# Kernel optimization log

Measured on AMD Instinct MI355X. Metric: run time of the kernel, lower is better.

Reference implementation:

```python
import jax, jax.numpy as jnp
import numpy as np

VOCAB = 100000
E = 300          # embedding_size
S = 128          # seq_len
B = 8192         # batch
H1 = 2048
H2 = 2048
C = 1221         # num_classes
PAD = 1          # padding token id (sentence trimmed after last non-1 token)


def setup_inputs() -> dict:
    key = jax.random.key(0)
    ks = jax.random.split(key, 8)
    x = jax.random.randint(ks[0], (S, B), 0, VOCAB, dtype=jnp.int64 if jax.config.jax_enable_x64 else jnp.int32)
    emb = jax.random.normal(ks[1], (VOCAB, E), dtype=jnp.float32) * 0.1
    W1 = jax.random.normal(ks[2], (H1, 2 * E), dtype=jnp.float32) * (1.0 / np.sqrt(2 * E))
    b1 = jnp.zeros((H1,), dtype=jnp.float32)
    W2 = jax.random.normal(ks[3], (H2, H1), dtype=jnp.float32) * (1.0 / np.sqrt(H1))
    b2 = jnp.zeros((H2,), dtype=jnp.float32)
    W_out = jax.random.normal(ks[4], (C, H2), dtype=jnp.float32) * (1.0 / np.sqrt(H2))
    b_out = jnp.zeros((C,), dtype=jnp.float32)
    return {"x": x, "emb": emb, "W1": W1, "b1": b1, "W2": W2, "b2": b2,
            "W_out": W_out, "b_out": b_out}


def reference(x, emb, W1, b1, W2, b2, W_out, b_out):
    # x: [S, B] token ids -> transpose to [B, S] as in torch forward
    xb = x.T                                   # [B, S]
    nonpad = xb != PAD                         # [B, S]
    # index of LAST non-padding token per sentence (torch: (sent != 1).nonzero()[-1])
    last = (S - 1) - jnp.argmax(nonpad[:, ::-1], axis=1)      # [B]
    pos = jnp.arange(S)
    # sentence[:last+1] keeps everything up to and including `last`,
    # including any PAD tokens inside that prefix (faithful to the slice).
    mask = (pos[None, :] <= last[:, None]).astype(emb.dtype)  # [B, S]

    ex = emb[xb]                               # [B, S, E] embedding lookup
    mean = jnp.einsum('bse,bs->be', ex, mask) / jnp.sum(mask, axis=1, keepdims=True)
    feat = jnp.concatenate([ex[:, 0, :], mean], axis=1)       # [B, 2E] (FEE + avg)

    h = jax.nn.relu(feat @ W1.T + b1)          # [B, H1]
    h = jax.nn.relu(h @ W2.T + b2)             # [B, H2]
    out = h @ W_out.T + b_out                  # [B, C]
    return out
```

## Files before the change

### kernel.cpp

```cpp
#include <hip/hip_runtime.h>
#include <hip/hip_bf16.h>

#define S 128
#define BATCH 8192
#define E 300
#define KPAD 640
#define H1 2048
#define H2 2048
#define CLS 1221
#define CPAD 1280
#define PADTOK 1
#define VOCAB 100000

typedef __bf16 bf16x8 __attribute__((ext_vector_type(8)));
typedef float f32x4 __attribute__((ext_vector_type(4)));

__device__ __forceinline__ float b2f(ushort u) {
  union { unsigned int i; float f; } v; v.i = ((unsigned int)u) << 16; return v.f;
}
__device__ __forceinline__ ushort f2b(float f) {
  unsigned int i = __float_as_uint(f);
  unsigned int r = (i + 0x7FFFu + ((i >> 16) & 1u)) >> 16;
  return (ushort)r;
}
__device__ __forceinline__ void async16(const void* g, void* l) {
  __builtin_amdgcn_global_load_lds(
      (__attribute__((address_space(1))) void*)(void*)(const_cast<void*>(g)),
      (__attribute__((address_space(3))) void*)l, 16, 0, 0);
}

#define NQ_EMB (VOCAB * E / 4)
#define NQ_W1  (H1 * KPAD / 4)
#define NQ_W2  (H1 * H2 / 4)
#define NQ_WO  (CPAD * H2 / 4)
#define NQ_XT  (S * BATCH / 4)
#define NQ_TOT (NQ_EMB + NQ_W1 + NQ_W2 + NQ_WO + NQ_XT)

__global__ __launch_bounds__(256) void cvt_all(const float* __restrict__ Ein,
                                               ushort* __restrict__ Eb,
                                               const float* __restrict__ W1,
                                               ushort* __restrict__ W1p,
                                               const float* __restrict__ W2,
                                               ushort* __restrict__ W2b,
                                               const float* __restrict__ Wout,
                                               ushort* __restrict__ Woutp,
                                               const int* __restrict__ x,
                                               int* __restrict__ xT) {
  int q = blockIdx.x * 256 + threadIdx.x;
  if (q < NQ_EMB) {
    float4 v = ((const float4*)Ein)[q];
    ushort4 o;
    o.x = f2b(v.x); o.y = f2b(v.y); o.z = f2b(v.z); o.w = f2b(v.w);
    ((ushort4*)Eb)[q] = o;
    return;
  }
  q -= NQ_EMB;
  if (q < NQ_W1) {
    int row = q / 160;
    int k0 = (q - row * 160) * 4;
    ushort4 o; o.x = 0; o.y = 0; o.z = 0; o.w = 0;
    if (k0 < 2 * E) {
      float4 v = *(const float4*)(W1 + (size_t)row * (2 * E) + k0);
      o.x = f2b(v.x); o.y = f2b(v.y); o.z = f2b(v.z); o.w = f2b(v.w);
    }
    ((ushort4*)W1p)[q] = o;
    return;
  }
  q -= NQ_W1;
  if (q < NQ_W2) {
    float4 v = ((const float4*)W2)[q];
    ushort4 o;
    o.x = f2b(v.x); o.y = f2b(v.y); o.z = f2b(v.z); o.w = f2b(v.w);
    ((ushort4*)W2b)[q] = o;
    return;
  }
  q -= NQ_W2;
  if (q < NQ_WO) {
    int n = (q * 4) >> 11;
    ushort4 o; o.x = 0; o.y = 0; o.z = 0; o.w = 0;
    if (n < CLS) {
      float4 v = ((const float4*)Wout)[q];
      o.x = f2b(v.x); o.y = f2b(v.y); o.z = f2b(v.z); o.w = f2b(v.w);
    }
    ((ushort4*)Woutp)[q] = o;
    return;
  }
  q -= NQ_WO;
  if (q < NQ_XT) {
    int b = q >> 5;
    int t4 = (q & 31) * 4;
    int4 o;
    o.x = x[(size_t)(t4 + 0) * BATCH + b];
    o.y = x[(size_t)(t4 + 1) * BATCH + b];
    o.z = x[(size_t)(t4 + 2) * BATCH + b];
    o.w = x[(size_t)(t4 + 3) * BATCH + b];
    ((int4*)xT)[q] = o;
  }
}

__global__ __launch_bounds__(128) void embed_kernel(const int* __restrict__ xT,
                                                    const ushort* __restrict__ emb,
                                                    ushort* __restrict__ feat) {
  __shared__ uint offs[S];
  __shared__ unsigned long long masks[2];
  __shared__ __align__(16) float part[76 * 4];
  const int b = blockIdx.x;
  const int t = threadIdx.x;

  int tok = xT[b * S + t];
  offs[t] = (uint)tok * 600u;
  unsigned long long m = __ballot(tok != PADTOK);
  if ((t & 63) == 0) masks[t >> 6] = m;
  __syncthreads();

  unsigned long long m0 = masks[0], m1 = masks[1];
  int last;
  if (m1)      last = 127 - __clzll(m1);
  else if (m0) last = 63 - __clzll(m0);
  else         last = S - 1;
  const int n = last + 1;
  const float inv = 1.0f / (float)n;

  const int w = t >> 6;
  const int lane = t & 63;
  const char* base = (const char*)emb;
  const uint off0 = (uint)lane * 8u;
  const bool tail = (lane < 11);
  const uint off1 = 512u + (uint)lane * 8u;

  float a0 = 0.f, a1 = 0.f, a2 = 0.f, a3 = 0.f;
  float c0 = 0.f, c1 = 0.f, c2 = 0.f, c3 = 0.f;

  int s = w;
  for (; s + 14 < n; s += 16) {
    uint o[8];
#pragma unroll
    for (int j = 0; j < 8; j++) o[j] = offs[s + 2 * j];
    ushort4 u[8];
#pragma unroll
    for (int j = 0; j < 8; j++) u[j] = *(const ushort4*)(base + (o[j] + off0));
    ushort4 v[8];
    if (tail) {
#pragma unroll
      for (int j = 0; j < 8; j++) v[j] = *(const ushort4*)(base + (o[j] + off1));
    }
#pragma unroll
    for (int j = 0; j < 8; j++) {
      a0 += b2f(u[j].x); a1 += b2f(u[j].y);
      a2 += b2f(u[j].z); a3 += b2f(u[j].w);
    }
    if (tail) {
#pragma unroll
      for (int j = 0; j < 8; j++) {
        c0 += b2f(v[j].x); c1 += b2f(v[j].y);
        c2 += b2f(v[j].z); c3 += b2f(v[j].w);
      }
    }
  }
  for (; s < n; s += 2) {
    uint o = offs[s];
    ushort4 u = *(const ushort4*)(base + (o + off0));
    a0 += b2f(u.x); a1 += b2f(u.y); a2 += b2f(u.z); a3 += b2f(u.w);
    if (tail) {
      ushort4 v = *(const ushort4*)(base + (o + off1));
      c0 += b2f(v.x); c1 += b2f(v.y); c2 += b2f(v.z); c3 += b2f(v.w);
    }
  }

  if (w == 1) {
    float4 av; av.x = a0; av.y = a1; av.z = a2; av.w = a3;
    *(float4*)&part[lane * 4] = av;
    if (tail) {
      float4 cv; cv.x = c0; cv.y = c1; cv.z = c2; cv.w = c3;
      *(float4*)&part[(64 + lane) * 4] = cv;
    }
  }
  __syncthreads();

  ushort* fr = feat + (size_t)b * KPAD;
  if (w == 0) {
    float4 pv = *(const float4*)&part[lane * 4];
    ushort4 mo;
    mo.x = f2b((a0 + pv.x) * inv); mo.y = f2b((a1 + pv.y) * inv);
    mo.z = f2b((a2 + pv.z) * inv); mo.w = f2b((a3 + pv.w) * inv);
    *(ushort4*)(fr + E + lane * 4) = mo;
    if (tail) {
      float4 qv = *(const float4*)&part[(64 + lane) * 4];
      ushort4 mo2;
      mo2.x = f2b((c0 + qv.x) * inv); mo2.y = f2b((c1 + qv.y) * inv);
      mo2.z = f2b((c2 + qv.z) * inv); mo2.w = f2b((c3 + qv.w) * inv);
      *(ushort4*)(fr + E + (64 + lane) * 4) = mo2;
    }
  }

  const uint o0 = offs[0];
  if (t < 75) {
    *(ushort4*)(fr + 4 * t) = *(const ushort4*)(base + (o0 + 8u * (uint)t));
  } else if (t < 85) {
    ushort4 z; z.x = 0; z.y = 0; z.z = 0; z.w = 0;
    *(ushort4*)(fr + 2 * E + 4 * (t - 75)) = z;
  }
}

#define BM 128
#define BN 128
#define BK 64

template <bool RELU, bool NGUARD, bool FP32OUT>
__global__ __launch_bounds__(256) void gemm_bt(const ushort* __restrict__ A,
                                               const ushort* __restrict__ B,
                                               const float* __restrict__ bias,
                                               void* __restrict__ Cv,
                                               int K, int lda, int ldb, int ldc,
                                               int Nreal) {
  __shared__ __align__(16) ushort lA[BM * BK];
  __shared__ __align__(16) ushort lB[BN * BK];

  const int tid = threadIdx.x;
  const int wave = tid >> 6;
  const int lane = tid & 63;
  const int m0 = blockIdx.y * BM;
  const int n0 = blockIdx.x * BN;
  const int wm = (wave >> 1) * 64;
  const int wn = (wave & 1) * 64;

  f32x4 acc[4][4];
#pragma unroll
  for (int i = 0; i < 4; i++)
#pragma unroll
    for (int j = 0; j < 4; j++)
#pragma unroll
      for (int r = 0; r < 4; r++) acc[i][j][r] = 0.f;

  const int srow8 = lane >> 3;
  const int kcw = (lane & 7) ^ srow8;

  const int fr = lane & 15;
  const int fq = lane >> 4;

  for (int k0 = 0; k0 < K; k0 += BK) {
#pragma unroll
    for (int j = 0; j < 4; j++) {
      const int g = wave * 4 + j;
      const int row = g * 8 + srow8;
      async16(A + (size_t)(m0 + row) * lda + k0 + kcw * 8, (void*)&lA[g * 512]);
      async16(B + (size_t)(n0 + row) * ldb + k0 + kcw * 8, (void*)&lB[g * 512]);
    }
    __syncthreads();

#pragma unroll
    for (int ks = 0; ks < 2; ks++) {
      const int kc = ks * 4 + fq;
      bf16x8 af[4], bfr[4];
#pragma unroll
      for (int mi = 0; mi < 4; mi++) {
        const int row = wm + mi * 16 + fr;
        af[mi] = *(const bf16x8*)&lA[(row * 8 + (kc ^ (row & 7))) * 8];
      }
#pragma unroll
      for (int ni = 0; ni < 4; ni++) {
        const int row = wn + ni * 16 + fr;
        bfr[ni] = *(const bf16x8*)&lB[(row * 8 + (kc ^ (row & 7))) * 8];
      }
#pragma unroll
      for (int mi = 0; mi < 4; mi++)
#pragma unroll
        for (int ni = 0; ni < 4; ni++)
          acc[mi][ni] = __builtin_amdgcn_mfma_f32_16x16x32_bf16(
              af[mi], bfr[ni], acc[mi][ni], 0, 0, 0);
    }
    __syncthreads();
  }

#pragma unroll
  for (int ni = 0; ni < 4; ni++) {
    const int col = n0 + wn + ni * 16 + fr;
    const bool ok = (!NGUARD) || (col < Nreal);
    const float bv = ok ? bias[col] : 0.f;
#pragma unroll
    for (int mi = 0; mi < 4; mi++) {
      const int rbase = m0 + wm + mi * 16 + fq * 4;
#pragma unroll
      for (int r = 0; r < 4; r++) {
        const int row = rbase + r;
        float v = acc[mi][ni][r] + bv;
        if (RELU) v = fmaxf(v, 0.f);
        if (ok) {
          if (FP32OUT) ((float*)Cv)[(size_t)row * ldc + col] = v;
          else         ((ushort*)Cv)[(size_t)row * ldc + col] = f2b(v);
        }
      }
    }
  }
}

extern "C" void kernel_launch(void* const* d_in, const int* in_sizes, int n_in,
                              void* d_out, int out_size, void* d_ws, size_t ws_size,
                              hipStream_t stream) {
  const int* x = (const int*)d_in[0];
  const float* emb = (const float*)d_in[1];
  const float* W1 = (const float*)d_in[2];
  const float* b1 = (const float*)d_in[3];
  const float* W2 = (const float*)d_in[4];
  const float* b2 = (const float*)d_in[5];
  const float* Wout = (const float*)d_in[6];
  const float* bout = (const float*)d_in[7];
  float* out = (float*)d_out;

  char* ws = (char*)d_ws;
  ushort* feat = (ushort*)ws;  ws += (size_t)BATCH * KPAD * 2;
  ushort* h1 = (ushort*)ws;    ws += (size_t)BATCH * H1 * 2;
  ushort* h2 = (ushort*)ws;    ws += (size_t)BATCH * H2 * 2;
  ushort* W1p = (ushort*)ws;   ws += (size_t)H1 * KPAD * 2;
  ushort* W2b = (ushort*)ws;   ws += (size_t)H2 * H1 * 2;
  ushort* Woutp = (ushort*)ws; ws += (size_t)CPAD * H2 * 2;
  ushort* Eb = (ushort*)ws;    ws += (size_t)VOCAB * E * 2;
  int* xT = (int*)ws;          ws += (size_t)S * BATCH * 4;

  cvt_all<<<(NQ_TOT + 255) / 256, 256, 0, stream>>>(emb, Eb, W1, W1p, W2, W2b,
                                                    Wout, Woutp, x, xT);
  embed_kernel<<<BATCH, S, 0, stream>>>(xT, Eb, feat);

  gemm_bt<true, false, false><<<dim3(H1 / BN, BATCH / BM), 256, 0, stream>>>(
      feat, W1p, b1, (void*)h1, KPAD, KPAD, KPAD, H1, H1);
  gemm_bt<true, false, false><<<dim3(H2 / BN, BATCH / BM), 256, 0, stream>>>(
      h1, W2b, b2, (void*)h2, H1, H1, H1, H2, H2);
  gemm_bt<false, true, true><<<dim3(CPAD / BN, BATCH / BM), 256, 0, stream>>>(
      h2, Woutp, bout, (void*)out, H2, H2, H2, CLS, CLS);
}
```

Before: 493.7 us.

## Rewrite GEMM as 256x256 tiles with double-buffered LDS and phased MFMA schedule

The bf16 GEMM kernel moves from 128x128 tiles with 4 waves and a single LDS buffer to 256x256 tiles with 8 waves and a double-buffered 128KB LDS. Global-to-LDS async loads for the next K tile are interleaved with MFMA phases, using explicit barriers, vmcnt waits and s_setprio. Workgroup IDs are remapped in groups of 8 for cache locality. The aim is to hide memory latency and raise arithmetic intensity. The cost is larger tiles that waste work on the padded 1280-column output GEMM and fewer workgroups, so the last wave of blocks may fill the GPU poorly.

```diff
diff --git a/kernel.cpp b/kernel.cpp
--- a/kernel.cpp
+++ b/kernel.cpp
@@ -202,88 +202,170 @@
   }
 }
 
-#define BM 128
-#define BN 128
-#define BK 64
+#define BM2 256
+#define BN2 256
+#define BK2 64
+
+__device__ __forceinline__ void stage_half(const ushort* __restrict__ P,
+                                           int ld, int org, ushort* dst,
+                                           int kg, int tid, int wave) {
+  const int sc = tid & 3;
+  const int r0 = tid >> 2;
+#pragma unroll
+  for (int j = 0; j < 2; ++j) {
+    const int row = j * 128 + r0;
+    const int c2 = sc ^ ((row >> 1) & 3);
+    async16(P + (size_t)(org + row) * ld + kg + c2 * 8,
+            (void*)(dst + j * 4096 + wave * 512));
+  }
+}
+
+#define PH_READ_B(KH)                                                        \
+  _Pragma("unroll") for (int nf = 0; nf < 4; ++nf) {                         \
+    const int row = wc * 64 + nf * 16 + fr;                                  \
+    bfrag[nf] = *(const bf16x8*)&sB[(KH) * 8192 + row * 32 +                 \
+                                    ((fq ^ ((row >> 1) & 3)) * 8)];          \
+  }
+#define PH_READ_A(MH, KH)                                                    \
+  _Pragma("unroll") for (int f = 0; f < 4; ++f) {                            \
+    const int row = wr * 128 + (MH) * 64 + f * 16 + fr;                      \
+    afrag[f] = *(const bf16x8*)&sA[(KH) * 8192 + row * 32 +                  \
+                                   ((fq ^ ((row >> 1) & 3)) * 8)];           \
+  }
+#define PH_MFMA(MH)                                                          \
+  __builtin_amdgcn_s_setprio(1);                                             \
+  _Pragma("unroll") for (int f = 0; f < 4; ++f)                              \
+    _Pragma("unroll") for (int nf = 0; nf < 4; ++nf)                         \
+      acc[(MH) * 4 + f][nf] = __builtin_amdgcn_mfma_f32_16x16x32_bf16(       \
+          afrag[f], bfrag[nf], acc[(MH) * 4 + f][nf], 0, 0, 0);              \
+  __builtin_amdgcn_s_setprio(0);
+#define BAR_SCHED()                                                          \
+  __builtin_amdgcn_s_barrier();                                              \
+  __builtin_amdgcn_sched_barrier(0);
 
 template <bool RELU, bool NGUARD, bool FP32OUT>
-__global__ __launch_bounds__(256) void gemm_bt(const ushort* __restrict__ A,
-                                               const ushort* __restrict__ B,
-                                               const float* __restrict__ bias,
-                                               void* __restrict__ Cv,
-                                               int K, int lda, int ldb, int ldc,
-                                               int Nreal) {
-  __shared__ __align__(16) ushort lA[BM * BK];
-  __shared__ __align__(16) ushort lB[BN * BK];
+__global__ __launch_bounds__(512, 2) void gemm_bt(const ushort* __restrict__ A,
+                                                  const ushort* __restrict__ B,
+                                                  const float* __restrict__ bias,
+                                                  void* __restrict__ Cv,
+                                                  int K, int lda, int ldb,
+                                                  int ldc, int Nreal) {
+  __shared__ __align__(16) ushort sm[65536];
 
   const int tid = threadIdx.x;
   const int wave = tid >> 6;
   const int lane = tid & 63;
-  const int m0 = blockIdx.y * BM;
-  const int n0 = blockIdx.x * BN;
-  const int wm = (wave >> 1) * 64;
-  const int wn = (wave & 1) * 64;
-
-  f32x4 acc[4][4];
-#pragma unroll
-  for (int i = 0; i < 4; i++)
-#pragma unroll
-    for (int j = 0; j < 4; j++)
-#pragma unroll
-      for (int r = 0; r < 4; r++) acc[i][j][r] = 0.f;
-
-  const int srow8 = lane >> 3;
-  const int kcw = (lane & 7) ^ srow8;
-
+
+  const int gx = gridDim.x;
+  const int nwg = gx * gridDim.y;
+  const int lin = blockIdx.y * gx + blockIdx.x;
+  const int wsw = (lin & 7) * (nwg >> 3) + (lin >> 3);
+  const int m0 = (wsw / gx) * BM2;
+  const int n0 = (wsw % gx) * BN2;
+
+  const int wr = wave >> 2;
+  const int wc = wave & 3;
   const int fr = lane & 15;
   const int fq = lane >> 4;
 
-  for (int k0 = 0; k0 < K; k0 += BK) {
-#pragma unroll
-    for (int j = 0; j < 4; j++) {
-      const int g = wave * 4 + j;
-      const int row = g * 8 + srow8;
-      async16(A + (size_t)(m0 + row) * lda + k0 + kcw * 8, (void*)&lA[g * 512]);
-      async16(B + (size_t)(n0 + row) * ldb + k0 + kcw * 8, (void*)&lB[g * 512]);
-    }
-    __syncthreads();
-
-#pragma unroll
-    for (int ks = 0; ks < 2; ks++) {
-      const int kc = ks * 4 + fq;
-      bf16x8 af[4], bfr[4];
-#pragma unroll
-      for (int mi = 0; mi < 4; mi++) {
-        const int row = wm + mi * 16 + fr;
-        af[mi] = *(const bf16x8*)&lA[(row * 8 + (kc ^ (row & 7))) * 8];
-      }
-#pragma unroll
-      for (int ni = 0; ni < 4; ni++) {
-        const int row = wn + ni * 16 + fr;
-        bfr[ni] = *(const bf16x8*)&lB[(row * 8 + (kc ^ (row & 7))) * 8];
-      }
-#pragma unroll
-      for (int mi = 0; mi < 4; mi++)
-#pragma unroll
-        for (int ni = 0; ni < 4; ni++)
-          acc[mi][ni] = __builtin_amdgcn_mfma_f32_16x16x32_bf16(
-              af[mi], bfr[ni], acc[mi][ni], 0, 0, 0);
-    }
-    __syncthreads();
-  }
-
-#pragma unroll
-  for (int ni = 0; ni < 4; ni++) {
-    const int col = n0 + wn + ni * 16 + fr;
+  f32x4 acc[8][4];
+#pragma unroll
+  for (int i = 0; i < 8; ++i)
+#pragma unroll
+    for (int j = 0; j < 4; ++j)
+#pragma unroll
+      for (int r = 0; r < 4; ++r) acc[i][j][r] = 0.f;
+
+  bf16x8 afrag[4], bfrag[4];
+  const int NT = K / BK2;
+
+  {
+    ushort* sA0 = sm;
+    ushort* sB0 = sm + 16384;
+    stage_half(A, lda, m0, sA0, 0, tid, wave);
+    stage_half(B, ldb, n0, sB0, 0, tid, wave);
+    stage_half(A, lda, m0, sA0 + 8192, 32, tid, wave);
+    stage_half(B, ldb, n0, sB0 + 8192, 32, tid, wave);
+    asm volatile("s_waitcnt vmcnt(4)" ::: "memory");
+    BAR_SCHED();
+  }
+
+  for (int t = 0; t < NT - 1; ++t) {
+    const int s = t & 1;
+    ushort* sA = sm + s * 32768;
+    ushort* sB = sA + 16384;
+    ushort* dA = sm + (s ^ 1) * 32768;
+    ushort* dB = dA + 16384;
+    const int kn = (t + 1) * BK2;
+
+    PH_READ_B(0);
+    PH_READ_A(0, 0);
+    stage_half(A, lda, m0, dA, kn, tid, wave);
+    BAR_SCHED();
+    PH_MFMA(0);
+    BAR_SCHED();
+
+    PH_READ_A(1, 0);
+    stage_half(B, ldb, n0, dB, kn, tid, wave);
+    asm volatile("s_waitcnt vmcnt(4)" ::: "memory");
+    BAR_SCHED();
+    PH_MFMA(1);
+    BAR_SCHED();
+
+    PH_READ_B(1);
+    PH_READ_A(0, 1);
+    stage_half(A, lda, m0, dA + 8192, kn + 32, tid, wave);
+    BAR_SCHED();
+    PH_MFMA(0);
+    BAR_SCHED();
+
+    PH_READ_A(1, 1);
+    stage_half(B, ldb, n0, dB + 8192, kn + 32, tid, wave);
+    asm volatile("s_waitcnt vmcnt(4)" ::: "memory");
+    BAR_SCHED();
+    PH_MFMA(1);
+    BAR_SCHED();
+  }
+
+  {
+    const int s = (NT - 1) & 1;
+    ushort* sA = sm + s * 32768;
+    ushort* sB = sA + 16384;
+
+    PH_READ_B(0);
+    PH_READ_A(0, 0);
+    BAR_SCHED();
+    PH_MFMA(0);
+    BAR_SCHED();
+
+    PH_READ_A(1, 0);
+    asm volatile("s_waitcnt vmcnt(0)" ::: "memory");
+    BAR_SCHED();
+    PH_MFMA(1);
+    BAR_SCHED();
+
+    PH_READ_B(1);
+    PH_READ_A(0, 1);
+    BAR_SCHED();
+    PH_MFMA(0);
+    BAR_SCHED();
+
+    PH_READ_A(1, 1);
+    PH_MFMA(1);
+  }
+
+#pragma unroll
+  for (int nf = 0; nf < 4; ++nf) {
+    const int col = n0 + wc * 64 + nf * 16 + fr;
     const bool ok = (!NGUARD) || (col < Nreal);
     const float bv = ok ? bias[col] : 0.f;
 #pragma unroll
-    for (int mi = 0; mi < 4; mi++) {
-      const int rbase = m0 + wm + mi * 16 + fq * 4;
-#pragma unroll
-      for (int r = 0; r < 4; r++) {
-        const int row = rbase + r;
-        float v = acc[mi][ni][r] + bv;
+    for (int g = 0; g < 8; ++g) {
+      const int rbase = m0 + wr * 128 + (g >> 2) * 64 + (g & 3) * 16 + fq * 4;
+#pragma unroll
+      for (int rr = 0; rr < 4; ++rr) {
+        const int row = rbase + rr;
+        float v = acc[g][nf][rr] + bv;
         if (RELU) v = fmaxf(v, 0.f);
         if (ok) {
           if (FP32OUT) ((float*)Cv)[(size_t)row * ldc + col] = v;
@@ -321,10 +403,10 @@
                                                     Wout, Woutp, x, xT);
   embed_kernel<<<BATCH, S, 0, stream>>>(xT, Eb, feat);
 
-  gemm_bt<true, false, false><<<dim3(H1 / BN, BATCH / BM), 256, 0, stream>>>(
+  gemm_bt<true, false, false><<<dim3(H1 / BN2, BATCH / BM2), 512, 0, stream>>>(
       feat, W1p, b1, (void*)h1, KPAD, KPAD, KPAD, H1, H1);
-  gemm_bt<true, false, false><<<dim3(H2 / BN, BATCH / BM), 256, 0, stream>>>(
+  gemm_bt<true, false, false><<<dim3(H2 / BN2, BATCH / BM2), 512, 0, stream>>>(
       h1, W2b, b2, (void*)h2, H1, H1, H1, H2, H2);
-  gemm_bt<false, true, true><<<dim3(CPAD / BN, BATCH / BM), 256, 0, stream>>>(
+  gemm_bt<false, true, true><<<dim3(CPAD / BN2, BATCH / BM2), 512, 0, stream>>>(
       h2, Woutp, bout, (void*)out, H2, H2, H2, CLS, CLS);
 }
```

Result: no change. 492.5 us (-0.2%).
